# Kernel optimization log

Measured on AMD Instinct MI355X. Metric: run time of the kernel, lower is better.

The kernel has to match this reference:

```python
import jax, jax.numpy as jnp
import numpy as np

N_NODES = 65536
N_EDGES = 1048576
IN_F = 128
HID_F = 128
OUT_F = 128


def setup_inputs() -> dict:
    key = jax.random.key(0)
    ks = jax.random.split(key, 8)
    feat = jax.random.normal(ks[0], (N_NODES, IN_F), dtype=jnp.float32)
    eweight = jax.random.uniform(ks[1], (N_EDGES, 1), dtype=jnp.float32)
    W1 = jax.random.normal(ks[2], (IN_F, HID_F), dtype=jnp.float32) * (1.0 / np.sqrt(IN_F))
    b1 = jnp.zeros((HID_F,), dtype=jnp.float32)
    W2 = jax.random.normal(ks[3], (HID_F, OUT_F), dtype=jnp.float32) * (1.0 / np.sqrt(HID_F))
    b2 = jnp.zeros((OUT_F,), dtype=jnp.float32)
    src = jax.random.randint(ks[4], (N_EDGES,), 0, N_NODES, dtype=jnp.int32)
    dst = jax.random.randint(ks[5], (N_EDGES,), 0, N_NODES, dtype=jnp.int32)
    return {"feat": feat, "eweight": eweight, "W1": W1, "b1": b1,
            "W2": W2, "b2": b2, "src": src, "dst": dst}


def _degrees(src, dst, n_nodes):
    ones = jnp.ones(src.shape[0], dtype=jnp.float32)
    deg_out = jax.ops.segment_sum(ones, src, num_segments=n_nodes)
    deg_in = jax.ops.segment_sum(ones, dst, num_segments=n_nodes)
    # DGL GraphConv clamps degree to min 1 before norm='both'
    return jnp.clip(deg_out, 1.0, None), jnp.clip(deg_in, 1.0, None)


def _graph_conv(feat, W, b, src, dst, out_norm, in_norm, n_nodes):
    # DGL GraphConv, norm='both': D_out^{-1/2} x -> x W -> spmm sum -> D_in^{-1/2} -> + b
    h = feat * out_norm[:, None]
    h = h @ W
    agg = jax.ops.segment_sum(h[src], dst, num_segments=n_nodes)
    return agg * in_norm[:, None] + b


def reference(feat, eweight, W1, b1, W2, b2, src, dst):
    n = feat.shape[0]
    deg_out, deg_in = _degrees(src, dst, n)
    out_norm = jax.lax.rsqrt(deg_out)
    in_norm = jax.lax.rsqrt(deg_in)
    h = _graph_conv(feat, W1, b1, src, dst, out_norm, in_norm, n)
    h = jax.nn.relu(h)
    h = _graph_conv(h, W2, b2, src, dst, out_norm, in_norm, n)
    # final update_all: u_mul_e + sum (eweight given)
    msg = h[src] * eweight  # [E, OUT_F]
    return jax.ops.segment_sum(msg, dst, num_segments=n)
```

## Files before the change

kernel.cpp:

```cpp
#include <hip/hip_runtime.h>

#define F 128
#define NN 65536
#define NBA 512
#define NBS 128
#define COARSE 256
#define CAP_BIN 4864
#define CAP_CSR 5632

typedef unsigned int uint;
typedef unsigned short ushort;
typedef unsigned char uchar;
typedef __attribute__((ext_vector_type(8))) short short8;
typedef __attribute__((ext_vector_type(8))) unsigned short ushort8;
typedef __attribute__((ext_vector_type(4))) float floatx4;

__device__ __forceinline__ ushort f2bf(float f) {
  uint u = __float_as_uint(f);
  u += 0x7fffu + ((u >> 16) & 1u);
  return (ushort)(u >> 16);
}


__global__ __launch_bounds__(256) void w_prep(const float* __restrict__ W1,
                                              const float* __restrict__ W2,
                                              ushort* __restrict__ W1t,
                                              ushort* __restrict__ W2t,
                                              int* __restrict__ cursorD,
                                              int* __restrict__ cursorS) {
  int b = blockIdx.x;
  if (b == 0) cursorD[threadIdx.x] = 0;
  if (b == 1) cursorS[threadIdx.x] = 0;
  const float* W = (b < 64) ? W1 : W2;
  ushort* Wt = (b < 64) ? W1t : W2t;
  int idx = (b & 63) * 256 + threadIdx.x;
  int k = idx >> 7, n = idx & 127;
  Wt[n * F + k] = f2bf(W[idx]);
}

__global__ __launch_bounds__(256) void bin_edges(
    const int* __restrict__ src, const int* __restrict__ dst,
    const float* __restrict__ ew, int E,
    int* __restrict__ cursorD, int* __restrict__ cursorS,
    uint2* __restrict__ slotD, uchar* __restrict__ srcF) {
  __shared__ int cnt[4][COARSE];
  __shared__ int base[COARSE];
  bool isD = blockIdx.x < NBA;
  int blk = isD ? blockIdx.x : blockIdx.x - NBA;
  int nblk = isD ? NBA : NBS;
  const int* key = isD ? dst : src;
  int* cursor = isD ? cursorD : cursorS;
  int wave = threadIdx.x >> 6;
  for (int i = threadIdx.x; i < 4 * COARSE; i += 256) ((int*)cnt)[i] = 0;
  __syncthreads();
  int chunk = (E + nblk - 1) / nblk;
  int s0 = blk * chunk, s1 = min(E, s0 + chunk);
  for (int i = s0 + threadIdx.x; i < s1; i += 256)
    atomicAdd(&cnt[wave][key[i] >> 8], 1);
  __syncthreads();
  if (threadIdx.x < COARSE) {
    int b = threadIdx.x;
    int tot = cnt[0][b] + cnt[1][b] + cnt[2][b] + cnt[3][b];
    base[b] = tot ? atomicAdd(&cursor[b], tot) : 0;
    cnt[0][b] = 0;
  }
  __syncthreads();
  if (isD) {
    for (int i = s0 + threadIdx.x; i < s1; i += 256) {
      int d = dst[i];
      int bin = d >> 8;
      int p = base[bin] + atomicAdd(&cnt[0][bin], 1);
      if (p < CAP_BIN) {
        uint2 v;
        v.x = (uint)(src[i] & 0xffff) | ((uint)f2bf(ew[i]) << 16);
        v.y = (uint)(d & 255);
        slotD[(size_t)bin * CAP_BIN + p] = v;
      }
    }
  } else {
    for (int i = s0 + threadIdx.x; i < s1; i += 256) {
      int s = src[i];
      int bin = s >> 8;
      int p = base[bin] + atomicAdd(&cnt[0][bin], 1);
      if (p < CAP_BIN) srcF[(size_t)bin * CAP_BIN + p] = (uchar)(s & 255);
    }
  }
}

__global__ __launch_bounds__(1024) void bucket_csr(
    const uint2* __restrict__ slotD, const int* __restrict__ cursorD,
    int2* __restrict__ rowRange, float* __restrict__ inNorm, uint* __restrict__ csr,
    const uchar* __restrict__ srcF, const int* __restrict__ cursorS,
    float* __restrict__ outNorm) {
  __shared__ int hist[256], base[256], cur[256];
  int t = threadIdx.x;
  if (blockIdx.x >= COARSE) {
    int b = blockIdx.x - COARSE;
    int lo = b * CAP_BIN;
    int cntS = min(cursorS[b], CAP_BIN);
    if (t < 256) hist[t] = 0;
    __syncthreads();
    for (int i = lo + t; i < lo + cntS; i += 1024)
      atomicAdd(&hist[srcF[i]], 1);
    __syncthreads();
    if (t < 256) outNorm[b * 256 + t] = rsqrtf((float)max(hist[t], 1));
    return;
  }
  int b = blockIdx.x;
  int lo = b * CAP_BIN;
  int cntD = min(cursorD[b], CAP_BIN);
  int hi = lo + cntD;
  if (t < 256) hist[t] = 0;
  __syncthreads();
  for (int i = lo + t; i < hi; i += 1024)
    atomicAdd(&hist[slotD[i].y], 1);
  __syncthreads();
  if (t < 256) base[t] = (hist[t] + 3) & ~3;
  __syncthreads();
  for (int off = 1; off < 256; off <<= 1) {
    int x = 0;
    if (t < 256 && t >= off) x = base[t - off];
    __syncthreads();
    if (t < 256) base[t] += x;
    __syncthreads();
  }
  if (t < 256) {
    int v = hist[t];
    int sz4 = (v + 3) & ~3;
    int st = b * CAP_CSR + base[t] - sz4;
    base[t] = st;
    cur[t] = 0;
    int node = b * 256 + t;
    rowRange[node] = make_int2(st, v);
    inNorm[node] = rsqrtf((float)max(v, 1));
    for (int p = st + v; p < st + sz4; ++p) csr[p] = 0x80000000u;
  }
  __syncthreads();
  for (int i = lo + t; i < hi; i += 1024) {
    uint2 v = slotD[i];
    int fine = v.y;
    int p = base[fine] + atomicAdd(&cur[fine], 1);
    csr[p] = v.x;
  }
}

template <bool BF16IN>
__global__ __launch_bounds__(256) void gemm_mfma(
    const void* __restrict__ Xv, const float* __restrict__ scale,
    const ushort* __restrict__ Wt, ushort* __restrict__ Y) {
  __shared__ ushort sA[128 * 136];
  __shared__ ushort sB[128 * 136];
  int t = threadIdx.x;
  int row0 = blockIdx.x * 128;

  {
    int r = t >> 1, hf = t & 1;
    ushort* ap = sA + r * 136 + hf * 64;
    if (BF16IN) {
      const ushort* xp = (const ushort*)Xv;
#pragma unroll
      for (int j = 0; j < 8; ++j) {
        int q = 2 * hf + (j >> 2);
        *(ushort8*)(ap + j * 8) =
            *(const ushort8*)(xp + ((size_t)q * NN + row0 + r) * 32 + (j & 3) * 8);
      }
    } else {
      const float* xp = (const float*)Xv + (size_t)(row0 + r) * F + hf * 64;
      float s = scale[row0 + r];
#pragma unroll
      for (int j = 0; j < 8; ++j) {
        float4 v0 = *(const float4*)(xp + j * 8);
        float4 v1 = *(const float4*)(xp + j * 8 + 4);
        ushort8 o;
        o[0] = f2bf(v0.x * s); o[1] = f2bf(v0.y * s); o[2] = f2bf(v0.z * s); o[3] = f2bf(v0.w * s);
        o[4] = f2bf(v1.x * s); o[5] = f2bf(v1.y * s); o[6] = f2bf(v1.z * s); o[7] = f2bf(v1.w * s);
        *(ushort8*)(ap + j * 8) = o;
      }
    }
  }
  {
    int n = t >> 1, hf = t & 1;
    const ushort* wp = Wt + n * F + hf * 64;
    ushort* bp = sB + n * 136 + hf * 64;
#pragma unroll
    for (int j = 0; j < 8; ++j)
      *(ushort8*)(bp + j * 8) = *(const ushort8*)(wp + j * 8);
  }
  __syncthreads();

  int lane = t & 63, wave = t >> 6;
  int quad = lane >> 4, l16 = lane & 15;
  int mrow0 = wave * 32;

  floatx4 acc[2][8];
#pragma unroll
  for (int a = 0; a < 2; ++a)
#pragma unroll
    for (int c = 0; c < 8; ++c) acc[a][c] = (floatx4){0.f, 0.f, 0.f, 0.f};

#pragma unroll
  for (int kc = 0; kc < 128; kc += 32) {
    short8 afrag[2], bfrag[8];
#pragma unroll
    for (int a = 0; a < 2; ++a)
      afrag[a] = *(const short8*)(sA + (mrow0 + a * 16 + l16) * 136 + kc + quad * 8);
#pragma unroll
    for (int c = 0; c < 8; ++c)
      bfrag[c] = *(const short8*)(sB + (c * 16 + l16) * 136 + kc + quad * 8);
#pragma unroll
    for (int a = 0; a < 2; ++a)
#pragma unroll
      for (int c = 0; c < 8; ++c)
        acc[a][c] = __builtin_amdgcn_mfma_f32_16x16x32_bf16(afrag[a], bfrag[c], acc[a][c], 0, 0, 0);
  }

#pragma unroll
  for (int a = 0; a < 2; ++a)
#pragma unroll
    for (int c = 0; c < 8; ++c)
#pragma unroll
      for (int r = 0; r < 4; ++r) {
        int row = row0 + mrow0 + a * 16 + quad * 4 + r;
        int col = c * 16 + l16;
        Y[((size_t)(col >> 5) * NN + row) * 32 + (col & 31)] = f2bf(acc[a][c][r]);
      }
}


template <bool EW, bool NB, bool RELU, bool PS, bool OUT_BF16>
__global__ __launch_bounds__(256) void spmm(
    const ushort* __restrict__ hb, const int2* __restrict__ rowRange,
    const uint* __restrict__ csr, const float* __restrict__ inNorm,
    const float* __restrict__ bias, const float* __restrict__ postScale,
    void* __restrict__ outv) {
  int bid = blockIdx.x;
  int plane = (bid & 7) >> 1;
  int chunk = ((bid >> 3) << 1) | (bid & 1);
  int lane = threadIdx.x & 63;
  int g = lane >> 2;
  int j = lane & 3;
  int n = chunk * 64 + (threadIdx.x >> 6) * 16 + g;
  int2 r = rowRange[n];
  int len4 = (r.y + 3) & ~3;
  const char* pb = (const char*)hb + (size_t)plane * ((size_t)NN * 64);
  uint joff = (uint)j << 4;
  float acc[8] = {0.f, 0.f, 0.f, 0.f, 0.f, 0.f, 0.f, 0.f};

#define GQ(e, c, q_)                                                     \
  {                                                                      \
    uint ei = (e);                                                       \
    c = *(const uint4*)(pb + (((ei & 0xffffu) << 6) | joff));            \
    q_ = EW ? __uint_as_float(ei & 0xffff0000u)                          \
            : ((int)ei >= 0 ? 1.0f : 0.0f);                              \
  }
#define ACC8(c, q_)                                                     \
  {                                                                     \
    acc[0] = fmaf(__uint_as_float(c.x << 16), q_, acc[0]);              \
    acc[1] = fmaf(__uint_as_float(c.x & 0xffff0000u), q_, acc[1]);      \
    acc[2] = fmaf(__uint_as_float(c.y << 16), q_, acc[2]);              \
    acc[3] = fmaf(__uint_as_float(c.y & 0xffff0000u), q_, acc[3]);      \
    acc[4] = fmaf(__uint_as_float(c.z << 16), q_, acc[4]);              \
    acc[5] = fmaf(__uint_as_float(c.z & 0xffff0000u), q_, acc[5]);      \
    acc[6] = fmaf(__uint_as_float(c.w << 16), q_, acc[6]);              \
    acc[7] = fmaf(__uint_as_float(c.w & 0xffff0000u), q_, acc[7]);      \
  }

  int i = 0;
  uint4 e0, e1;
  if (i + 8 <= len4) {
    e0 = *(const uint4*)(csr + r.x);
    e1 = *(const uint4*)(csr + r.x + 4);
  }
  while (i + 8 <= len4) {
    uint4 c0, c1, c2, c3, c4, c5, c6, c7;
    float q0, q1, q2, q3, q4, q5, q6, q7;
    GQ(e0.x, c0, q0) GQ(e0.y, c1, q1) GQ(e0.z, c2, q2) GQ(e0.w, c3, q3)
    GQ(e1.x, c4, q4) GQ(e1.y, c5, q5) GQ(e1.z, c6, q6) GQ(e1.w, c7, q7)
    uint4 f0, f1;
    bool more = (i + 16 <= len4);
    if (more) {
      f0 = *(const uint4*)(csr + r.x + i + 8);
      f1 = *(const uint4*)(csr + r.x + i + 12);
    }
    ACC8(c0, q0) ACC8(c1, q1) ACC8(c2, q2) ACC8(c3, q3)
    ACC8(c4, q4) ACC8(c5, q5) ACC8(c6, q6) ACC8(c7, q7)
    if (more) { e0 = f0; e1 = f1; }
    i += 8;
  }
  if (i < len4) {
    uint4 t0 = *(const uint4*)(csr + r.x + i);
    uint4 c0, c1, c2, c3;
    float q0, q1, q2, q3;
    GQ(t0.x, c0, q0) GQ(t0.y, c1, q1) GQ(t0.z, c2, q2) GQ(t0.w, c3, q3)
    ACC8(c0, q0) ACC8(c1, q1) ACC8(c2, q2) ACC8(c3, q3)
  }
#undef GQ
#undef ACC8

  if (NB) {
    float sc = inNorm[n];
    float4 b0 = ((const float4*)bias)[plane * 8 + j * 2];
    float4 b1 = ((const float4*)bias)[plane * 8 + j * 2 + 1];
    float bb[8] = {b0.x, b0.y, b0.z, b0.w, b1.x, b1.y, b1.z, b1.w};
#pragma unroll
    for (int k = 0; k < 8; ++k) {
      acc[k] = fmaf(acc[k], sc, bb[k]);
      if (RELU) acc[k] = fmaxf(acc[k], 0.f);
    }
    if (PS) {
      float o = postScale[n];
#pragma unroll
      for (int k = 0; k < 8; ++k) acc[k] *= o;
    }
  }
  if (OUT_BF16) {
    uint4 o;
    o.x = ((uint)f2bf(acc[1]) << 16) | (uint)f2bf(acc[0]);
    o.y = ((uint)f2bf(acc[3]) << 16) | (uint)f2bf(acc[2]);
    o.z = ((uint)f2bf(acc[5]) << 16) | (uint)f2bf(acc[4]);
    o.w = ((uint)f2bf(acc[7]) << 16) | (uint)f2bf(acc[6]);
    ((uint4*)outv)[((size_t)plane * NN + n) * 4 + j] = o;
  } else {
    float4 lo = {acc[0], acc[1], acc[2], acc[3]};
    float4 hi = {acc[4], acc[5], acc[6], acc[7]};
    ((float4*)outv)[(size_t)n * 32 + plane * 8 + j * 2] = lo;
    ((float4*)outv)[(size_t)n * 32 + plane * 8 + j * 2 + 1] = hi;
  }
}


extern "C" void kernel_launch(void* const* d_in, const int* in_sizes, int n_in,
                              void* d_out, int out_size, void* d_ws, size_t ws_size,
                              hipStream_t stream) {
  const float* feat = (const float*)d_in[0];
  const float* ew   = (const float*)d_in[1];
  const float* W1   = (const float*)d_in[2];
  const float* b1   = (const float*)d_in[3];
  const float* W2   = (const float*)d_in[4];
  const float* b2   = (const float*)d_in[5];
  const int*   src  = (const int*)d_in[6];
  const int*   dst  = (const int*)d_in[7];
  const int N = in_sizes[0] / F;
  const int E = in_sizes[6];
  float* out = (float*)d_out;

  char* ws = (char*)d_ws;
  size_t off = 0;
  auto alloc = [&](size_t bytes) {
    void* p = ws + off;
    off += (bytes + 255) & ~(size_t)255;
    return p;
  };
  int2*   rowRange = (int2*)alloc((size_t)N * 8);
  float*  inNorm   = (float*)alloc((size_t)N * 4);
  float*  outNorm  = (float*)alloc((size_t)N * 4);
  ushort* W1t      = (ushort*)alloc((size_t)F * F * 2);
  ushort* W2t      = (ushort*)alloc((size_t)F * F * 2);
  int*    cursorD  = (int*)alloc(COARSE * 4);
  int*    cursorS  = (int*)alloc(COARSE * 4);
  uint*   csr      = (uint*)alloc((size_t)COARSE * CAP_CSR * 4);
  ushort* bufAb    = (ushort*)alloc((size_t)N * F * 2);
  ushort* bufBb    = (ushort*)alloc((size_t)N * F * 2);
  ushort* bufCb    = (ushort*)alloc((size_t)N * F * 2);
  if (off > ws_size) return;

  uint2* slotD;
  uchar* srcF;
  {
    char* tp = (char*)bufBb;
    size_t toff = 0;
    auto talloc = [&](size_t bytes) {
      void* p = tp + toff;
      toff += (bytes + 255) & ~(size_t)255;
      return p;
    };
    slotD = (uint2*)talloc((size_t)COARSE * CAP_BIN * 8);
    srcF  = (uchar*)talloc((size_t)COARSE * CAP_BIN);
  }

  w_prep<<<128, 256, 0, stream>>>(W1, W2, W1t, W2t, cursorD, cursorS);
  bin_edges<<<NBA + NBS, 256, 0, stream>>>(src, dst, ew, E, cursorD, cursorS, slotD, srcF);
  bucket_csr<<<2 * COARSE, 1024, 0, stream>>>(slotD, cursorD, rowRange, inNorm, csr,
                                              srcF, cursorS, outNorm);

  gemm_mfma<false><<<N / 128, 256, 0, stream>>>(feat, outNorm, W1t, bufAb);
  spmm<false, true, true, true, true><<<N / 16, 256, 0, stream>>>(
      bufAb, rowRange, csr, inNorm, b1, outNorm, bufBb);
  gemm_mfma<true><<<N / 128, 256, 0, stream>>>(bufBb, nullptr, W2t, bufAb);
  spmm<false, true, false, false, true><<<N / 16, 256, 0, stream>>>(
      bufAb, rowRange, csr, inNorm, b2, nullptr, bufCb);
  spmm<true, false, false, false, false><<<N / 16, 256, 0, stream>>>(
      bufCb, rowRange, csr, nullptr, nullptr, nullptr, out);
}
```

Baseline: 259.1 us.

## Fuse first-layer SpMM with second-layer GEMM through shared memory

Adds a spmm_gemm kernel in which each 512-thread block aggregates 128 rows of layer-1 features (norm, bias, ReLU, post-scale), stages the bf16 result in LDS, then multiplies by W2 with MFMA and writes the layer-2 input directly. This drops one kernel launch and the global write and re-read of the intermediate hidden matrix. In exchange, the block-level sync makes the GEMM wait for the slowest row gather, and the gather now uses fewer, larger blocks, which may lower occupancy and latency hiding for the irregular loads. The W2 fragments are read from global memory by every block.

```diff
diff --git a/kernel.cpp b/kernel.cpp
--- a/kernel.cpp
+++ b/kernel.cpp
@@ -226,6 +226,122 @@
       }
 }
 
+
+__global__ __launch_bounds__(512) void spmm_gemm(
+    const ushort* __restrict__ hb, const int2* __restrict__ rowRange,
+    const uint* __restrict__ csr, const float* __restrict__ inNorm,
+    const float* __restrict__ bias, const float* __restrict__ postScale,
+    const ushort* __restrict__ Wt, ushort* __restrict__ Y) {
+  __shared__ ushort sA[128 * 136];
+  int t = threadIdx.x;
+  int w = t >> 6;
+  int lane = t & 63;
+  int g = lane >> 2;
+  int j = lane & 3;
+  int row0 = blockIdx.x * 128;
+  uint joff = (uint)j << 4;
+
+#define GQ(e, c, q_)                                                     \
+  {                                                                      \
+    uint ei = (e);                                                       \
+    c = *(const uint4*)(pb + (((ei & 0xffffu) << 6) | joff));            \
+    q_ = ((int)ei >= 0 ? 1.0f : 0.0f);                                   \
+  }
+#define ACC8(c, q_)                                                     \
+  {                                                                     \
+    acc[0] = fmaf(__uint_as_float(c.x << 16), q_, acc[0]);              \
+    acc[1] = fmaf(__uint_as_float(c.x & 0xffff0000u), q_, acc[1]);      \
+    acc[2] = fmaf(__uint_as_float(c.y << 16), q_, acc[2]);              \
+    acc[3] = fmaf(__uint_as_float(c.y & 0xffff0000u), q_, acc[3]);      \
+    acc[4] = fmaf(__uint_as_float(c.z << 16), q_, acc[4]);              \
+    acc[5] = fmaf(__uint_as_float(c.z & 0xffff0000u), q_, acc[5]);      \
+    acc[6] = fmaf(__uint_as_float(c.w << 16), q_, acc[6]);              \
+    acc[7] = fmaf(__uint_as_float(c.w & 0xffff0000u), q_, acc[7]);      \
+  }
+
+  for (int s = 0; s < 4; ++s) {
+    int unit = s * 8 + w;
+    int ng = unit >> 2;
+    int plane = unit & 3;
+    int n = row0 + ng * 16 + g;
+    const char* pb = (const char*)hb + (size_t)plane * ((size_t)NN * 64);
+    int2 r = rowRange[n];
+    int len4 = (r.y + 3) & ~3;
+    float acc[8] = {0.f, 0.f, 0.f, 0.f, 0.f, 0.f, 0.f, 0.f};
+
+    int i = 0;
+    uint4 e0, e1;
+    if (8 <= len4) {
+      e0 = *(const uint4*)(csr + r.x);
+      e1 = *(const uint4*)(csr + r.x + 4);
+    }
+    while (i + 8 <= len4) {
+      uint4 c0, c1, c2, c3, c4, c5, c6, c7;
+      float q0, q1, q2, q3, q4, q5, q6, q7;
+      GQ(e0.x, c0, q0) GQ(e0.y, c1, q1) GQ(e0.z, c2, q2) GQ(e0.w, c3, q3)
+      GQ(e1.x, c4, q4) GQ(e1.y, c5, q5) GQ(e1.z, c6, q6) GQ(e1.w, c7, q7)
+      uint4 f0, f1;
+      bool more = (i + 16 <= len4);
+      if (more) {
+        f0 = *(const uint4*)(csr + r.x + i + 8);
+        f1 = *(const uint4*)(csr + r.x + i + 12);
+      }
+      ACC8(c0, q0) ACC8(c1, q1) ACC8(c2, q2) ACC8(c3, q3)
+      ACC8(c4, q4) ACC8(c5, q5) ACC8(c6, q6) ACC8(c7, q7)
+      if (more) { e0 = f0; e1 = f1; }
+      i += 8;
+    }
+    if (i < len4) {
+      uint4 t0 = *(const uint4*)(csr + r.x + i);
+      uint4 c0, c1, c2, c3;
+      float q0, q1, q2, q3;
+      GQ(t0.x, c0, q0) GQ(t0.y, c1, q1) GQ(t0.z, c2, q2) GQ(t0.w, c3, q3)
+      ACC8(c0, q0) ACC8(c1, q1) ACC8(c2, q2) ACC8(c3, q3)
+    }
+
+    float sc = inNorm[n];
+    float4 b0 = ((const float4*)bias)[plane * 8 + j * 2];
+    float4 b1v = ((const float4*)bias)[plane * 8 + j * 2 + 1];
+    float bb[8] = {b0.x, b0.y, b0.z, b0.w, b1v.x, b1v.y, b1v.z, b1v.w};
+    float o = postScale[n];
+    ushort8 ov;
+#pragma unroll
+    for (int k = 0; k < 8; ++k) {
+      float v = fmaf(acc[k], sc, bb[k]);
+      v = fmaxf(v, 0.f) * o;
+      ov[k] = f2bf(v);
+    }
+    *(ushort8*)(sA + (ng * 16 + g) * 136 + plane * 32 + j * 8) = ov;
+  }
+#undef GQ
+#undef ACC8
+  __syncthreads();
+
+  int quad = lane >> 4, l16 = lane & 15;
+  int mrow0 = w * 16;
+  floatx4 gacc[8];
+#pragma unroll
+  for (int c = 0; c < 8; ++c) gacc[c] = (floatx4){0.f, 0.f, 0.f, 0.f};
+#pragma unroll
+  for (int kc = 0; kc < 128; kc += 32) {
+    short8 afrag = *(const short8*)(sA + (mrow0 + l16) * 136 + kc + quad * 8);
+    short8 bfrag[8];
+#pragma unroll
+    for (int c = 0; c < 8; ++c)
+      bfrag[c] = *(const short8*)(Wt + (c * 16 + l16) * F + kc + quad * 8);
+#pragma unroll
+    for (int c = 0; c < 8; ++c)
+      gacc[c] = __builtin_amdgcn_mfma_f32_16x16x32_bf16(afrag, bfrag[c], gacc[c], 0, 0, 0);
+  }
+#pragma unroll
+  for (int c = 0; c < 8; ++c)
+#pragma unroll
+    for (int r4 = 0; r4 < 4; ++r4) {
+      int row = row0 + mrow0 + quad * 4 + r4;
+      int col = c * 16 + l16;
+      Y[((size_t)(col >> 5) * NN + row) * 32 + (col & 31)] = f2bf(gacc[c][r4]);
+    }
+}
 
 template <bool EW, bool NB, bool RELU, bool PS, bool OUT_BF16>
 __global__ __launch_bounds__(256) void spmm(
@@ -384,11 +500,10 @@
                                               srcF, cursorS, outNorm);
 
   gemm_mfma<false><<<N / 128, 256, 0, stream>>>(feat, outNorm, W1t, bufAb);
-  spmm<false, true, true, true, true><<<N / 16, 256, 0, stream>>>(
-      bufAb, rowRange, csr, inNorm, b1, outNorm, bufBb);
-  gemm_mfma<true><<<N / 128, 256, 0, stream>>>(bufBb, nullptr, W2t, bufAb);
+  spmm_gemm<<<N / 128, 512, 0, stream>>>(
+      bufAb, rowRange, csr, inNorm, b1, outNorm, W2t, bufBb);
   spmm<false, true, false, false, true><<<N / 16, 256, 0, stream>>>(
-      bufAb, rowRange, csr, inNorm, b2, nullptr, bufCb);
+      bufBb, rowRange, csr, inNorm, b2, nullptr, bufCb);
   spmm<true, false, false, false, false><<<N / 16, 256, 0, stream>>>(
       bufCb, rowRange, csr, nullptr, nullptr, nullptr, out);
 }
```

New measurement: 286.5 us. 1.11x slower.
